# Kernel tuning notes

Hardware: AMD Instinct MI355X
Metric: run time of the kernel (lower is better)

Reference implementation:

```python
import jax, jax.numpy as jnp
import numpy as np

B, S, D, H = 2, 2048, 1024, 16
HD = D // H  # 64


def setup_inputs() -> dict:
    key = jax.random.key(0)
    ks = jax.random.split(key, 7)
    scale = 1.0 / np.sqrt(D)
    return {
        "embeddings": jax.random.normal(ks[0], (B, S, D), dtype=jnp.float32),
        "W_kv": jax.random.uniform(ks[1], (D, 2 * D), jnp.float32, -scale, scale),
        "b_kv": jax.random.uniform(ks[2], (2 * D,), jnp.float32, -scale, scale),
        "W_q": jax.random.uniform(ks[3], (D, D), jnp.float32, -scale, scale),
        "b_q": jax.random.uniform(ks[4], (D,), jnp.float32, -scale, scale),
        "W_o": jax.random.uniform(ks[5], (D, D), jnp.float32, -scale, scale),
        "b_o": jax.random.uniform(ks[6], (D,), jnp.float32, -scale, scale),
    }


def reference(embeddings, W_kv, b_kv, W_q, b_q, W_o, b_o):
    # kv projection -> [B, S, H, 2*HD] -> [B, H, S, 2*HD]
    kv = (embeddings @ W_kv + b_kv).reshape(B, S, H, 2 * HD).transpose(0, 2, 1, 3)
    q = (embeddings @ W_q + b_q).reshape(B, S, H, HD).transpose(0, 2, 1, 3)
    k, v = kv[..., :HD], kv[..., HD:]
    # naive scaled dot-product attention (full [B,H,S,S] score matrix)
    scores = jnp.einsum("bhqd,bhkd->bhqk", q, k) / jnp.sqrt(jnp.float32(HD))
    attn = jax.nn.softmax(scores, axis=-1)
    ctx = jnp.einsum("bhqk,bhkd->bhqd", attn, v)  # [B,H,S,HD]
    ctx = ctx.transpose(0, 2, 1, 3).reshape(B, S, D)
    return ctx @ W_o + b_o
```

## Files before the change

kernel.cpp:

```cpp
#include <hip/hip_runtime.h>
#include <hip/hip_bf16.h>


typedef unsigned short ushort;
typedef __attribute__((ext_vector_type(4))) float f32x4;
typedef __attribute__((ext_vector_type(16))) float f32x16;
typedef __attribute__((ext_vector_type(8))) __bf16 bf16x8;
typedef __attribute__((ext_vector_type(8))) unsigned short u16x8;
typedef __attribute__((ext_vector_type(4))) unsigned short u16x4;
typedef __attribute__((ext_vector_type(4))) unsigned int u32x4;

#define LOG2E 1.44269504088896340736f

constexpr int Bc = 2, Sc = 2048, Dc = 1024, Hc = 16, HDc = 64;

__device__ inline ushort f2bf(float f) {
    unsigned u = __builtin_bit_cast(unsigned, f);
    u += 0x7fffu + ((u >> 16) & 1u);
    return (ushort)(u >> 16);
}

__device__ inline float fexp2(float x) {
#if __has_builtin(__builtin_amdgcn_exp2f)
    return __builtin_amdgcn_exp2f(x);
#else
    return exp2f(x);
#endif
}

__device__ inline void gload16(const void* g, void* l) {
    __builtin_amdgcn_global_load_lds((const __attribute__((address_space(1))) void*)g,
                                     (__attribute__((address_space(3))) void*)l, 16, 0, 0);
}

__device__ inline f32x4 mfma16(bf16x8 a, bf16x8 b, f32x4 c) {
    return __builtin_amdgcn_mfma_f32_16x16x32_bf16(a, b, c, 0, 0, 0);
}
__device__ inline f32x16 mfma32(bf16x8 a, bf16x8 b, f32x16 c) {
    return __builtin_amdgcn_mfma_f32_32x32x16_bf16(a, b, c, 0, 0, 0);
}
__device__ inline unsigned cvtpk(float lo, float hi_) {
    unsigned r; asm("v_cvt_pk_bf16_f32 %0, %1, %2" : "=v"(r) : "v"(lo), "v"(hi_)); return r;
}
__device__ inline void swap32(unsigned& a, unsigned& b) {
    asm("v_permlane32_swap_b32 %0, %1" : "+v"(a), "+v"(b));
}

__global__ __launch_bounds__(256) void prep_k(const float* __restrict__ emb,
                                              ushort* __restrict__ embb,
                                              const float* __restrict__ Wkv,
                                              const float* __restrict__ Wq,
                                              const float* __restrict__ Wo,
                                              ushort* __restrict__ WtAll) {
    const int bid = blockIdx.x;
    if (bid < 2048) {
        int i = bid * 256 + threadIdx.x;
        const float4* p = (const float4*)emb;
        float4 a = p[2 * i], b = p[2 * i + 1];
        u16x8 r;
        r[0] = f2bf(a.x); r[1] = f2bf(a.y); r[2] = f2bf(a.z); r[3] = f2bf(a.w);
        r[4] = f2bf(b.x); r[5] = f2bf(b.y); r[6] = f2bf(b.z); r[7] = f2bf(b.w);
        ((u16x8*)embb)[i] = r;
        return;
    }
    __shared__ float t[32][33];
    int tb = bid - 2048;
    const float* W; int N, rowofs;
    if (tb < 2048)      { W = Wkv; N = 2048; rowofs = 0; }
    else if (tb < 3072) { W = Wq;  N = 1024; rowofs = 2048; tb -= 2048; }
    else                { W = Wo;  N = 1024; rowofs = 3072; tb -= 3072; }
    const int nbx = N >> 5;
    const int bx = tb % nbx, by = tb / nbx;
    const int tx = threadIdx.x & 31, ty = threadIdx.x >> 5;
    const int bj = bx * 32, bi = by * 32;
#pragma unroll
    for (int i = 0; i < 4; i++) {
        int r = ty + i * 8;
        t[r][tx] = W[(size_t)(bi + r) * N + bj + tx];
    }
    __syncthreads();
#pragma unroll
    for (int i = 0; i < 4; i++) {
        int r = ty + i * 8;
        WtAll[(size_t)(rowofs + bj + r) * 1024 + bi + tx] = f2bf(t[tx][r]);
    }
}

template <int MODE>
__global__ __launch_bounds__(256) void gemm_bt_k(const ushort* __restrict__ A,
                                                 const ushort* __restrict__ Bt,
                                                 const float* __restrict__ bias,
                                                 const float* __restrict__ bias2,
                                                 void* __restrict__ Cout,
                                                 ushort* __restrict__ Vout,
                                                 ushort* __restrict__ Qout,
                                                 int M, int N, int K) {
    __shared__ __align__(16) char sA[2][8192];
    __shared__ __align__(16) char sB[2][8192];
    const int tid = threadIdx.x;
    const int nbc = N >> 7;
    const int cpx = (gridDim.x >> 3);
    const int swzb = (blockIdx.x & 7) * cpx + (blockIdx.x >> 3);
    const int brow = swzb / nbc, bcol = swzb % nbc;
    const int w = tid >> 6, lane = tid & 63;
    const int wr = w >> 1, wc = w & 1;
    const int lg = lane >> 4, l16 = lane & 15;

    f32x4 acc[4][4] = {};

    const int r0 = tid >> 2;
    const int sl = (tid & 3) ^ (r0 & 3);
    const ushort* a0 = A + (size_t)(brow * 128 + r0) * K + sl * 8;
    const ushort* a1 = A + (size_t)(brow * 128 + 64 + r0) * K + sl * 8;
    const ushort* b0 = Bt + (size_t)(bcol * 128 + r0) * K + sl * 8;
    const ushort* b1 = Bt + (size_t)(bcol * 128 + 64 + r0) * K + sl * 8;

    const int arow = wr * 64 + l16;
    const int bcolr = wc * 64 + l16;

    auto STAGE = [&](int buf, int k0) {
        gload16(a0 + k0, sA[buf] + w * 1024);
        gload16(a1 + k0, sA[buf] + 4096 + w * 1024);
        gload16(b0 + k0, sB[buf] + w * 1024);
        gload16(b1 + k0, sB[buf] + 4096 + w * 1024);
    };

    const int nk = K >> 5;
    STAGE(0, 0);

    for (int k0 = 0; k0 < nk; k0++) {
        const int buf = k0 & 1;
        if (k0 < nk - 1) {
            STAGE(buf ^ 1, (k0 + 1) << 5);
            asm volatile("s_waitcnt vmcnt(4)" ::: "memory");
        } else {
            asm volatile("s_waitcnt vmcnt(0)" ::: "memory");
        }
        __builtin_amdgcn_s_barrier();
        __builtin_amdgcn_sched_barrier(0);

        bf16x8 af[4], bfr[4];
#pragma unroll
        for (int rf = 0; rf < 4; rf++) {
            int rr = arow + rf * 16;
            af[rf] = *(const bf16x8*)(sA[buf] + rr * 64 + ((lg * 16) ^ ((rr & 3) << 4)));
        }
#pragma unroll
        for (int cf = 0; cf < 4; cf++) {
            int rr = bcolr + cf * 16;
            bfr[cf] = *(const bf16x8*)(sB[buf] + rr * 64 + ((lg * 16) ^ ((rr & 3) << 4)));
        }
#pragma unroll
        for (int rf = 0; rf < 4; rf++)
#pragma unroll
            for (int cf = 0; cf < 4; cf++)
                acc[rf][cf] = mfma16(af[rf], bfr[cf], acc[rf][cf]);
        __builtin_amdgcn_s_barrier();
    }

#pragma unroll
    for (int cf = 0; cf < 4; cf++) {
        const int col = bcol * 128 + wc * 64 + cf * 16 + l16;
        if constexpr (MODE == 3) {
            if (col < 2048) {
                const float bv = bias[col];
                const int h = col >> 7, lo = col & 127;
#pragma unroll
                for (int rf = 0; rf < 4; rf++) {
                    int row = brow * 128 + wr * 64 + rf * 16 + lg * 4;
                    int b = row >> 11, s = row & 2047;
                    if (lo < 64) {
                        ushort* Kout = (ushort*)Cout;
#pragma unroll
                        for (int r = 0; r < 4; r++)
                            Kout[((size_t)(b * 16 + h) * 2048 + s + r) * 64 + lo] =
                                f2bf(acc[rf][cf][r] + bv);
                    } else {
                        u16x4 pk;
#pragma unroll
                        for (int r = 0; r < 4; r++) pk[r] = f2bf(acc[rf][cf][r] + bv);
                        *(u16x4*)(Vout + ((size_t)(b * 16 + h) * 64 + (lo - 64)) * 2048 + s) = pk;
                    }
                }
            } else {
                const int qc = col - 2048;
                const float bv = bias2[qc];
                const float qs = 0.125f * LOG2E;
#pragma unroll
                for (int rf = 0; rf < 4; rf++) {
                    int row = brow * 128 + wr * 64 + rf * 16 + lg * 4;
#pragma unroll
                    for (int r = 0; r < 4; r++)
                        Qout[(size_t)(row + r) * 1024 + qc] =
                            f2bf((acc[rf][cf][r] + bv) * qs);
                }
            }
        } else {
            const float bv = bias[col];
#pragma unroll
            for (int rf = 0; rf < 4; rf++) {
                int row = brow * 128 + wr * 64 + rf * 16 + lg * 4;
#pragma unroll
                for (int r = 0; r < 4; r++) {
                    float v = acc[rf][cf][r] + bv;
                    if (MODE == 1) ((float*)Cout)[(size_t)(row + r) * N + col] = v;
                    else           ((ushort*)Cout)[(size_t)(row + r) * N + col] = f2bf(v);
                }
            }
        }
    }
}

__global__ __launch_bounds__(256, 4) void attn2_k(const ushort* __restrict__ Qg,
                                                  const ushort* __restrict__ Kg,
                                                  const ushort* __restrict__ Vg,
                                                  ushort* __restrict__ ctx) {
    __shared__ __align__(16) char sK[2][8192];
    __shared__ __align__(16) char sV[2][8192];
    const int tid = threadIdx.x;
    const int wg = ((blockIdx.x & 7) << 7) | (blockIdx.x >> 3);
    const int bh = wg >> 5, qt = wg & 31;
    const int b = bh >> 4, h = bh & 15;
    const int w = tid >> 6, lane = tid & 63;
    const int ql = lane & 31, hi = lane >> 5;
    const int ksub = w & 1;
    const int qhalf = w >> 1;

    const ushort* Kh = Kg + (size_t)bh * (Sc * 64);
    const ushort* Vh = Vg + (size_t)bh * (64 * Sc);

    const int qrow = qt * 64 + qhalf * 32 + ql;
    bf16x8 qf[4];
    {
        const ushort* qp = Qg + ((size_t)(b * Sc + qrow)) * Dc + h * HDc + hi * 8;
#pragma unroll
        for (int jd = 0; jd < 4; jd++) qf[jd] = *(const bf16x8*)(qp + jd * 16);
    }

    const u16x8 ones_u = {0x3F80, 0x3F80, 0x3F80, 0x3F80, 0x3F80, 0x3F80, 0x3F80, 0x3F80};
    const bf16x8 ones8 = __builtin_bit_cast(bf16x8, ones_u);

    const int rw = w * 16 + (lane >> 3);
    const int sl = (lane & 7) ^ (lane >> 3);

    f32x16 o0 = {}, o1 = {}, ls = {};
    const float MH = 8.0f * LOG2E;
    const int sw = (ql & 7) << 4;

    auto STAGE = [&](int buf, int kt) {
#pragma unroll
        for (int j = 0; j < 2; j++) {
            gload16(Kh + (size_t)(kt * 64 + rw + 8 * j) * 64 + sl * 8,
                    sK[buf] + w * 2048 + j * 1024);
            gload16(Vh + (size_t)(rw + 8 * j) * Sc + kt * 64 + sl * 8,
                    sV[buf] + w * 2048 + j * 1024);
        }
    };

    int cur = 0;
    STAGE(0, 0);

    constexpr int NT = Sc / 64;
    for (int kt = 0; kt < NT; kt++) {
        if (kt < NT - 1) {
            STAGE(cur ^ 1, kt + 1);
            asm volatile("s_waitcnt vmcnt(4)" ::: "memory");
        } else {
            asm volatile("s_waitcnt vmcnt(0)" ::: "memory");
        }
        __builtin_amdgcn_s_barrier();
        __builtin_amdgcn_sched_barrier(0);

        f32x16 st;
        {
            f32x16 a;
#pragma unroll
            for (int i = 0; i < 16; i++) a[i] = -MH;
            const char* kb = sK[cur] + (ksub * 32 + ql) * 128;
            __builtin_amdgcn_s_setprio(1);
#pragma unroll
            for (int jd = 0; jd < 4; jd++) {
                bf16x8 kf = *(const bf16x8*)(kb + ((jd * 32 + hi * 16) ^ sw));
                a = mfma32(kf, qf[jd], a);
            }
            __builtin_amdgcn_s_setprio(0);
            st = a;
        }

#pragma unroll
        for (int i = 0; i < 16; i++) st[i] = fexp2(st[i]);

        {
            unsigned a0 = cvtpk(st[0],  st[1]);
            unsigned a1 = cvtpk(st[2],  st[3]);
            unsigned a2 = cvtpk(st[4],  st[5]);
            unsigned a3 = cvtpk(st[6],  st[7]);
            swap32(a0, a2); swap32(a1, a3);
            u32x4 f0v = {a0, a1, a2, a3};
            bf16x8 pf0 = __builtin_bit_cast(bf16x8, f0v);
            unsigned c0 = cvtpk(st[8],  st[9]);
            unsigned c1 = cvtpk(st[10], st[11]);
            unsigned c2 = cvtpk(st[12], st[13]);
            unsigned c3 = cvtpk(st[14], st[15]);
            swap32(c0, c2); swap32(c1, c3);
            u32x4 f1v = {c0, c1, c2, c3};
            bf16x8 pf1 = __builtin_bit_cast(bf16x8, f1v);

            const char* vb0 = sV[cur] + ql * 128;
            const char* vb1 = sV[cur] + (32 + ql) * 128;
            bf16x8 vf;
            __builtin_amdgcn_s_setprio(1);
            vf = *(const bf16x8*)(vb0 + ((ksub * 64 +  0 + hi * 16) ^ sw)); o0 = mfma32(vf, pf0, o0);
            vf = *(const bf16x8*)(vb0 + ((ksub * 64 + 32 + hi * 16) ^ sw)); o0 = mfma32(vf, pf1, o0);
            vf = *(const bf16x8*)(vb1 + ((ksub * 64 +  0 + hi * 16) ^ sw)); o1 = mfma32(vf, pf0, o1);
            vf = *(const bf16x8*)(vb1 + ((ksub * 64 + 32 + hi * 16) ^ sw)); o1 = mfma32(vf, pf1, o1);
            ls = mfma32(ones8, pf0, ls);
            ls = mfma32(ones8, pf1, ls);
            __builtin_amdgcn_s_setprio(0);
        }
        __builtin_amdgcn_s_barrier();
        cur ^= 1;
    }

    float l_run = ls[0];

    __syncthreads();
    float* ox = (float*)sK;
    float* lx = (float*)sV;
    if (ksub) {
        const int base = qhalf * 2048;
#pragma unroll
        for (int i = 0; i < 16; i++) {
            ox[base + i * 64 + lane] = o0[i];
            ox[base + (16 + i) * 64 + lane] = o1[i];
        }
        lx[qhalf * 64 + lane] = l_run;
    }
    __syncthreads();
    if (!ksub) {
        const int base = qhalf * 2048;
#pragma unroll
        for (int i = 0; i < 16; i++) {
            o0[i] += ox[base + i * 64 + lane];
            o1[i] += ox[base + (16 + i) * 64 + lane];
        }
        l_run += lx[qhalf * 64 + lane];
        const float inv = 1.0f / l_run;
        ushort* cp = ctx + ((size_t)(b * Sc + qrow)) * Dc + h * HDc;
#pragma unroll
        for (int g = 0; g < 4; g++) {
            u16x4 pk0, pk1;
#pragma unroll
            for (int r = 0; r < 4; r++) {
                pk0[r] = f2bf(o0[g * 4 + r] * inv);
                pk1[r] = f2bf(o1[g * 4 + r] * inv);
            }
            *(u16x4*)(cp + g * 8 + hi * 4) = pk0;
            *(u16x4*)(cp + 32 + g * 8 + hi * 4) = pk1;
        }
    }
}

extern "C" void kernel_launch(void* const* d_in, const int* in_sizes, int n_in,
                              void* d_out, int out_size, void* d_ws, size_t ws_size,
                              hipStream_t stream) {
    const float* emb  = (const float*)d_in[0];
    const float* W_kv = (const float*)d_in[1];
    const float* b_kv = (const float*)d_in[2];
    const float* W_q  = (const float*)d_in[3];
    const float* b_q  = (const float*)d_in[4];
    const float* W_o  = (const float*)d_in[5];
    const float* b_o  = (const float*)d_in[6];
    float* out = (float*)d_out;

    const int BS = Bc * Sc;
    ushort* embb  = (ushort*)d_ws;
    ushort* wallt = embb  + (size_t)BS * Dc;
    ushort* wot   = wallt + (size_t)3 * Dc * Dc;
    ushort* Kb    = wallt + (size_t)4 * Dc * Dc;
    ushort* Vtb   = Kb    + (size_t)32 * Sc * HDc;
    ushort* Qb    = Vtb   + (size_t)32 * Sc * HDc;
    ushort* ctxb  = Qb    + (size_t)BS * Dc;

    prep_k<<<6144, 256, 0, stream>>>(emb, embb, W_kv, W_q, W_o, wallt);

    gemm_bt_k<3><<<(BS / 128) * (3072 / 128), 256, 0, stream>>>(
        embb, wallt, b_kv, b_q, Kb, Vtb, Qb, BS, 3072, Dc);

    attn2_k<<<Bc * Hc * (Sc / 64), 256, 0, stream>>>(Qb, Kb, Vtb, ctxb);

    gemm_bt_k<1><<<(BS / 128) * (Dc / 128), 256, 0, stream>>>(
        ctxb, wot, b_o, nullptr, out, nullptr, nullptr, BS, Dc, Dc);
}
```

Baseline: 117.5 us.

## Double attention query tile per block to reuse K/V tiles across more queries

Each attention workgroup now handles 128 query rows instead of 64, with each wave computing two 32-row query groups against the same K and V fragments loaded from LDS. This halves the grid and the global/LDS traffic for K and V per query, raising the MFMA-to-load ratio. In exchange, register pressure roughly doubles, so launch bounds drop to 2 waves per SIMD, and the block count falls to 512, which lowers occupancy and latency hiding.

After: 115.0 us. 2.1% less time.

```diff
diff --git a/kernel.cpp b/kernel.cpp
--- a/kernel.cpp
+++ b/kernel.cpp
@@ -211,30 +211,32 @@
     }
 }
 
-__global__ __launch_bounds__(256, 4) void attn2_k(const ushort* __restrict__ Qg,
+__global__ __launch_bounds__(256, 2) void attn2_k(const ushort* __restrict__ Qg,
                                                   const ushort* __restrict__ Kg,
                                                   const ushort* __restrict__ Vg,
                                                   ushort* __restrict__ ctx) {
     __shared__ __align__(16) char sK[2][8192];
     __shared__ __align__(16) char sV[2][8192];
+    __shared__ float lx2[256];
     const int tid = threadIdx.x;
-    const int wg = ((blockIdx.x & 7) << 7) | (blockIdx.x >> 3);
-    const int bh = wg >> 5, qt = wg & 31;
+    const int wg = ((blockIdx.x & 7) << 6) | (blockIdx.x >> 3);
+    const int bh = wg >> 4, qt = wg & 15;
     const int b = bh >> 4, h = bh & 15;
     const int w = tid >> 6, lane = tid & 63;
     const int ql = lane & 31, hi = lane >> 5;
     const int ksub = w & 1;
-    const int qhalf = w >> 1;
+    const int qq = w >> 1;
 
     const ushort* Kh = Kg + (size_t)bh * (Sc * 64);
     const ushort* Vh = Vg + (size_t)bh * (64 * Sc);
 
-    const int qrow = qt * 64 + qhalf * 32 + ql;
-    bf16x8 qf[4];
-    {
-        const ushort* qp = Qg + ((size_t)(b * Sc + qrow)) * Dc + h * HDc + hi * 8;
-#pragma unroll
-        for (int jd = 0; jd < 4; jd++) qf[jd] = *(const bf16x8*)(qp + jd * 16);
+    const int qrow0 = qt * 128 + qq * 64 + ql;
+    bf16x8 qf[2][4];
+#pragma unroll
+    for (int qg = 0; qg < 2; qg++) {
+        const ushort* qp = Qg + ((size_t)(b * Sc + qrow0 + qg * 32)) * Dc + h * HDc + hi * 8;
+#pragma unroll
+        for (int jd = 0; jd < 4; jd++) qf[qg][jd] = *(const bf16x8*)(qp + jd * 16);
     }
 
     const u16x8 ones_u = {0x3F80, 0x3F80, 0x3F80, 0x3F80, 0x3F80, 0x3F80, 0x3F80, 0x3F80};
@@ -243,7 +245,8 @@
     const int rw = w * 16 + (lane >> 3);
     const int sl = (lane & 7) ^ (lane >> 3);
 
-    f32x16 o0 = {}, o1 = {}, ls = {};
+    f32x16 o[2][2] = {};
+    f32x16 ls[2] = {};
     const float MH = 8.0f * LOG2E;
     const int sw = (ql & 7) << 4;
 
@@ -271,92 +274,113 @@
         __builtin_amdgcn_s_barrier();
         __builtin_amdgcn_sched_barrier(0);
 
-        f32x16 st;
+        bf16x8 kf[4];
         {
-            f32x16 a;
-#pragma unroll
-            for (int i = 0; i < 16; i++) a[i] = -MH;
             const char* kb = sK[cur] + (ksub * 32 + ql) * 128;
-            __builtin_amdgcn_s_setprio(1);
-#pragma unroll
-            for (int jd = 0; jd < 4; jd++) {
-                bf16x8 kf = *(const bf16x8*)(kb + ((jd * 32 + hi * 16) ^ sw));
-                a = mfma32(kf, qf[jd], a);
-            }
-            __builtin_amdgcn_s_setprio(0);
-            st = a;
-        }
-
-#pragma unroll
-        for (int i = 0; i < 16; i++) st[i] = fexp2(st[i]);
-
-        {
-            unsigned a0 = cvtpk(st[0],  st[1]);
-            unsigned a1 = cvtpk(st[2],  st[3]);
-            unsigned a2 = cvtpk(st[4],  st[5]);
-            unsigned a3 = cvtpk(st[6],  st[7]);
+#pragma unroll
+            for (int jd = 0; jd < 4; jd++)
+                kf[jd] = *(const bf16x8*)(kb + ((jd * 32 + hi * 16) ^ sw));
+        }
+
+        f32x16 st[2];
+#pragma unroll
+        for (int qg = 0; qg < 2; qg++)
+#pragma unroll
+            for (int i = 0; i < 16; i++) st[qg][i] = -MH;
+        __builtin_amdgcn_s_setprio(1);
+#pragma unroll
+        for (int qg = 0; qg < 2; qg++)
+#pragma unroll
+            for (int jd = 0; jd < 4; jd++)
+                st[qg] = mfma32(kf[jd], qf[qg][jd], st[qg]);
+        __builtin_amdgcn_s_setprio(0);
+
+#pragma unroll
+        for (int qg = 0; qg < 2; qg++)
+#pragma unroll
+            for (int i = 0; i < 16; i++) st[qg][i] = fexp2(st[qg][i]);
+
+        bf16x8 pf[2][2];
+#pragma unroll
+        for (int qg = 0; qg < 2; qg++) {
+            unsigned a0 = cvtpk(st[qg][0],  st[qg][1]);
+            unsigned a1 = cvtpk(st[qg][2],  st[qg][3]);
+            unsigned a2 = cvtpk(st[qg][4],  st[qg][5]);
+            unsigned a3 = cvtpk(st[qg][6],  st[qg][7]);
             swap32(a0, a2); swap32(a1, a3);
             u32x4 f0v = {a0, a1, a2, a3};
-            bf16x8 pf0 = __builtin_bit_cast(bf16x8, f0v);
-            unsigned c0 = cvtpk(st[8],  st[9]);
-            unsigned c1 = cvtpk(st[10], st[11]);
-            unsigned c2 = cvtpk(st[12], st[13]);
-            unsigned c3 = cvtpk(st[14], st[15]);
+            pf[qg][0] = __builtin_bit_cast(bf16x8, f0v);
+            unsigned c0 = cvtpk(st[qg][8],  st[qg][9]);
+            unsigned c1 = cvtpk(st[qg][10], st[qg][11]);
+            unsigned c2 = cvtpk(st[qg][12], st[qg][13]);
+            unsigned c3 = cvtpk(st[qg][14], st[qg][15]);
             swap32(c0, c2); swap32(c1, c3);
             u32x4 f1v = {c0, c1, c2, c3};
-            bf16x8 pf1 = __builtin_bit_cast(bf16x8, f1v);
-
-            const char* vb0 = sV[cur] + ql * 128;
-            const char* vb1 = sV[cur] + (32 + ql) * 128;
-            bf16x8 vf;
-            __builtin_amdgcn_s_setprio(1);
-            vf = *(const bf16x8*)(vb0 + ((ksub * 64 +  0 + hi * 16) ^ sw)); o0 = mfma32(vf, pf0, o0);
-            vf = *(const bf16x8*)(vb0 + ((ksub * 64 + 32 + hi * 16) ^ sw)); o0 = mfma32(vf, pf1, o0);
-            vf = *(const bf16x8*)(vb1 + ((ksub * 64 +  0 + hi * 16) ^ sw)); o1 = mfma32(vf, pf0, o1);
-            vf = *(const bf16x8*)(vb1 + ((ksub * 64 + 32 + hi * 16) ^ sw)); o1 = mfma32(vf, pf1, o1);
-            ls = mfma32(ones8, pf0, ls);
-            ls = mfma32(ones8, pf1, ls);
-            __builtin_amdgcn_s_setprio(0);
-        }
+            pf[qg][1] = __builtin_bit_cast(bf16x8, f1v);
+        }
+
+        bf16x8 vf[2][2];
+#pragma unroll
+        for (int dg = 0; dg < 2; dg++) {
+            const char* vb = sV[cur] + (dg * 32 + ql) * 128;
+#pragma unroll
+            for (int ks = 0; ks < 2; ks++)
+                vf[dg][ks] = *(const bf16x8*)(vb + ((ksub * 64 + ks * 32 + hi * 16) ^ sw));
+        }
+
+        __builtin_amdgcn_s_setprio(1);
+#pragma unroll
+        for (int qg = 0; qg < 2; qg++)
+#pragma unroll
+            for (int ks = 0; ks < 2; ks++) {
+                o[0][qg] = mfma32(vf[0][ks], pf[qg][ks], o[0][qg]);
+                o[1][qg] = mfma32(vf[1][ks], pf[qg][ks], o[1][qg]);
+                ls[qg]   = mfma32(ones8,     pf[qg][ks], ls[qg]);
+            }
+        __builtin_amdgcn_s_setprio(0);
+
         __builtin_amdgcn_s_barrier();
         cur ^= 1;
     }
 
-    float l_run = ls[0];
-
     __syncthreads();
-    float* ox = (float*)sK;
-    float* lx = (float*)sV;
+    float* ox = qq ? (float*)sV : (float*)sK;
     if (ksub) {
-        const int base = qhalf * 2048;
-#pragma unroll
-        for (int i = 0; i < 16; i++) {
-            ox[base + i * 64 + lane] = o0[i];
-            ox[base + (16 + i) * 64 + lane] = o1[i];
-        }
-        lx[qhalf * 64 + lane] = l_run;
+#pragma unroll
+        for (int dg = 0; dg < 2; dg++)
+#pragma unroll
+            for (int qg = 0; qg < 2; qg++)
+#pragma unroll
+                for (int i = 0; i < 16; i++)
+                    ox[((dg * 2 + qg) * 16 + i) * 64 + lane] = o[dg][qg][i];
+        lx2[(qq * 2 + 0) * 64 + lane] = ls[0][0];
+        lx2[(qq * 2 + 1) * 64 + lane] = ls[1][0];
     }
     __syncthreads();
     if (!ksub) {
-        const int base = qhalf * 2048;
-#pragma unroll
-        for (int i = 0; i < 16; i++) {
-            o0[i] += ox[base + i * 64 + lane];
-            o1[i] += ox[base + (16 + i) * 64 + lane];
-        }
-        l_run += lx[qhalf * 64 + lane];
-        const float inv = 1.0f / l_run;
-        ushort* cp = ctx + ((size_t)(b * Sc + qrow)) * Dc + h * HDc;
-#pragma unroll
-        for (int g = 0; g < 4; g++) {
-            u16x4 pk0, pk1;
-#pragma unroll
-            for (int r = 0; r < 4; r++) {
-                pk0[r] = f2bf(o0[g * 4 + r] * inv);
-                pk1[r] = f2bf(o1[g * 4 + r] * inv);
-            }
-            *(u16x4*)(cp + g * 8 + hi * 4) = pk0;
-            *(u16x4*)(cp + 32 + g * 8 + hi * 4) = pk1;
+#pragma unroll
+        for (int dg = 0; dg < 2; dg++)
+#pragma unroll
+            for (int qg = 0; qg < 2; qg++)
+#pragma unroll
+                for (int i = 0; i < 16; i++)
+                    o[dg][qg][i] += ox[((dg * 2 + qg) * 16 + i) * 64 + lane];
+        const float inv0 = 1.0f / (ls[0][0] + lx2[(qq * 2 + 0) * 64 + lane]);
+        const float inv1 = 1.0f / (ls[1][0] + lx2[(qq * 2 + 1) * 64 + lane]);
+#pragma unroll
+        for (int qg = 0; qg < 2; qg++) {
+            const float inv = qg ? inv1 : inv0;
+            ushort* cp = ctx + ((size_t)(b * Sc + qrow0 + qg * 32)) * Dc + h * HDc;
+#pragma unroll
+            for (int dg = 0; dg < 2; dg++)
+#pragma unroll
+                for (int g = 0; g < 4; g++) {
+                    u16x4 pk;
+#pragma unroll
+                    for (int r = 0; r < 4; r++)
+                        pk[r] = f2bf(o[dg][qg][g * 4 + r] * inv);
+                    *(u16x4*)(cp + dg * 32 + g * 8 + hi * 4) = pk;
+                }
         }
     }
 }
@@ -387,7 +411,7 @@
     gemm_bt_k<3><<<(BS / 128) * (3072 / 128), 256, 0, stream>>>(
         embb, wallt, b_kv, b_q, Kb, Vtb, Qb, BS, 3072, Dc);
 
-    attn2_k<<<Bc * Hc * (Sc / 64), 256, 0, stream>>>(Qb, Kb, Vtb, ctxb);
+    attn2_k<<<Bc * Hc * (Sc / 128), 256, 0, stream>>>(Qb, Kb, Vtb, ctxb);
 
     gemm_bt_k<1><<<(BS / 128) * (Dc / 128), 256, 0, stream>>>(
         ctxb, wot, b_o, nullptr, out, nullptr, nullptr, BS, Dc, Dc);
```
